# Performance work log

Measured on AMD Instinct MI355X. Metric: run time of the kernel, lower is better.

Reference implementation:

```python
import jax, jax.numpy as jnp
import numpy as np

ATT_SIZE = 32
HEAD_NUM = 2


def setup_inputs() -> dict:
    key = jax.random.key(0)
    k_in, k_q, k_k, k_v, k_r = jax.random.split(key, 5)
    B, F, D = 16384, 32, 64
    H = ATT_SIZE * HEAD_NUM  # 64
    inputs = jax.random.normal(k_in, (B, F, D), dtype=jnp.float32)
    W_Query = jax.random.truncated_normal(k_q, -2.0, 2.0, (D, H), dtype=jnp.float32) * 0.05
    W_Key = jax.random.truncated_normal(k_k, -2.0, 2.0, (D, H), dtype=jnp.float32) * 0.05
    W_Value = jax.random.truncated_normal(k_v, -2.0, 2.0, (D, H), dtype=jnp.float32) * 0.05
    W_Res = jax.random.truncated_normal(k_r, -2.0, 2.0, (D, H), dtype=jnp.float32) * 0.05
    return {"inputs": inputs, "W_Query": W_Query, "W_Key": W_Key, "W_Value": W_Value, "W_Res": W_Res}


def reference(inputs, W_Query, W_Key, W_Value, W_Res):
    B, F, D = inputs.shape
    h, a = HEAD_NUM, ATT_SIZE
    # project and reshape to [B, h, F, a]
    q = jnp.einsum('bfd,de->bfe', inputs, W_Query).reshape(B, F, h, a).transpose(0, 2, 1, 3)
    k = jnp.einsum('bfd,de->bfe', inputs, W_Key).reshape(B, F, h, a).transpose(0, 2, 1, 3)
    v = jnp.einsum('bfd,de->bfe', inputs, W_Value).reshape(B, F, h, a).transpose(0, 2, 1, 3)
    # NOTE: original code has NO 1/sqrt(d) scaling
    scores = jnp.einsum('bhqa,bhka->bhqk', q, k)
    attn = jax.nn.softmax(scores, axis=-1)
    out = jnp.einsum('bhqk,bhka->bhqa', attn, v)  # [B, h, F, a]
    out = out.transpose(0, 2, 1, 3).reshape(B, F, h * a)
    out = out + jnp.einsum('bfd,de->bfe', inputs, W_Res)
    return jax.nn.relu(out)
```

## Files before the change

kernel.cpp:

```cpp
#include <hip/hip_runtime.h>


constexpr int kF = 32, kD = 64, kH = 64;

constexpr int XS = 72;
constexpr int QS = 72;
constexpr int VS = 40;
constexpr int PS = 40;

using short8   = __attribute__((ext_vector_type(8))) short;
using float4v  = __attribute__((ext_vector_type(4))) float;
using ushort4v = __attribute__((ext_vector_type(4))) unsigned short;

__device__ __forceinline__ unsigned short f2bf(float x) {
    return __builtin_bit_cast(unsigned short, (__bf16)x);
}
__device__ __forceinline__ float bf2f(unsigned short b) {
    return __uint_as_float((unsigned)b << 16);
}

__global__ void wprep_kernel(const float* __restrict__ Wq, const float* __restrict__ Wk,
                             const float* __restrict__ Wv, const float* __restrict__ Wr,
                             unsigned short* __restrict__ wt) {
    const int m = blockIdx.x;
    const float* __restrict__ W = (m == 0) ? Wq : (m == 1) ? Wk : (m == 2) ? Wv : Wr;
    for (int i = threadIdx.x; i < kD * kH; i += blockDim.x) {
        const int e = i >> 6, d = i & 63;
        wt[m * kD * kH + e * kD + d] = f2bf(W[d * kH + e]);
    }
}

__global__ __launch_bounds__(256)
void interact_mfma(const float* __restrict__ X, const unsigned short* __restrict__ Wt,
                   float* __restrict__ out)
{
    __shared__ __align__(16) unsigned short s_xp[2 * kF * PS];
    __shared__ __align__(16) unsigned short s_q [kF * QS];
    __shared__ __align__(16) unsigned short s_k [kF * QS];
    __shared__ __align__(16) unsigned short s_vt[kH * VS];
    __shared__ __align__(16) unsigned short s_rt[kH * VS];

    const int t    = threadIdx.x;
    const int w    = t >> 6;
    const int lane = t & 63;
    const int quad = lane >> 4;
    const int l    = lane & 15;
    const int b    = blockIdx.x;

    short8 bfrag[4][2];
    {
        const unsigned short* __restrict__ wtm = Wt + w * (kD * kH);
        #pragma unroll
        for (int nt = 0; nt < 4; ++nt)
            #pragma unroll
            for (int ks = 0; ks < 2; ++ks)
                bfrag[nt][ks] =
                    *reinterpret_cast<const short8*>(wtm + (16 * nt + l) * kD + 32 * ks + quad * 8);
    }

    const float* __restrict__ Xb = X + (size_t)b * (kF * kD);
    #pragma unroll
    for (int i = 0; i < 2; ++i) {
        const int idx = i * 256 + t;
        const int f = idx >> 4, c = idx & 15;
        const float4 v = reinterpret_cast<const float4*>(Xb)[idx];
        ushort4v pk = { f2bf(v.x), f2bf(v.y), f2bf(v.z), f2bf(v.w) };
        *reinterpret_cast<ushort4v*>(&s_xp[f * XS + c * 4]) = pk;
    }
    __syncthreads();

    {
        float4v acc[2][4];
        #pragma unroll
        for (int mt = 0; mt < 2; ++mt)
            #pragma unroll
            for (int nt = 0; nt < 4; ++nt)
                acc[mt][nt] = (float4v){0.f, 0.f, 0.f, 0.f};

        short8 afrag[2][2];
        #pragma unroll
        for (int mt = 0; mt < 2; ++mt)
            #pragma unroll
            for (int ks = 0; ks < 2; ++ks)
                afrag[mt][ks] =
                    *reinterpret_cast<const short8*>(&s_xp[(16 * mt + l) * XS + 32 * ks + quad * 8]);

        #pragma unroll
        for (int mt = 0; mt < 2; ++mt)
            #pragma unroll
            for (int nt = 0; nt < 4; ++nt) {
                acc[mt][nt] = __builtin_amdgcn_mfma_f32_16x16x32_bf16(
                    afrag[mt][0], bfrag[nt][0], acc[mt][nt], 0, 0, 0);
                acc[mt][nt] = __builtin_amdgcn_mfma_f32_16x16x32_bf16(
                    afrag[mt][1], bfrag[nt][1], acc[mt][nt], 0, 0, 0);
            }

        if (w < 2) {
            unsigned short* __restrict__ dst = (w == 0) ? s_q : s_k;
            #pragma unroll
            for (int mt = 0; mt < 2; ++mt)
                #pragma unroll
                for (int nt = 0; nt < 4; ++nt)
                    #pragma unroll
                    for (int r = 0; r < 4; ++r)
                        dst[(16 * mt + quad * 4 + r) * QS + 16 * nt + l] = f2bf(acc[mt][nt][r]);
        } else {
            unsigned short* __restrict__ dstT = (w == 2) ? s_vt : s_rt;
            #pragma unroll
            for (int mt = 0; mt < 2; ++mt)
                #pragma unroll
                for (int nt = 0; nt < 4; ++nt) {
                    ushort4v pk = { f2bf(acc[mt][nt][0]), f2bf(acc[mt][nt][1]),
                                    f2bf(acc[mt][nt][2]), f2bf(acc[mt][nt][3]) };
                    *reinterpret_cast<ushort4v*>(
                        &dstT[(16 * nt + l) * VS + 16 * mt + 4 * quad]) = pk;
                }
        }
    }
    __syncthreads();

    const int h  = w >> 1;
    const int mt = w & 1;
    float inv[4];
    {
        const short8 qa =
            *reinterpret_cast<const short8*>(&s_q[(16 * mt + l) * QS + 32 * h + quad * 8]);
        const short8 kb0 =
            *reinterpret_cast<const short8*>(&s_k[(l) * QS + 32 * h + quad * 8]);
        const short8 kb1 =
            *reinterpret_cast<const short8*>(&s_k[(16 + l) * QS + 32 * h + quad * 8]);

        float4v s0 = (float4v){0.f, 0.f, 0.f, 0.f};
        float4v s1 = (float4v){0.f, 0.f, 0.f, 0.f};
        s0 = __builtin_amdgcn_mfma_f32_16x16x32_bf16(qa, kb0, s0, 0, 0, 0);
        s1 = __builtin_amdgcn_mfma_f32_16x16x32_bf16(qa, kb1, s1, 0, 0, 0);

        #pragma unroll
        for (int r = 0; r < 4; ++r) {
            float m = fmaxf(s0[r], s1[r]);
            #pragma unroll
            for (int d = 1; d < 16; d <<= 1) m = fmaxf(m, __shfl_xor(m, d));
            const float e0 = __expf(s0[r] - m);
            const float e1 = __expf(s1[r] - m);
            float sum = e0 + e1;
            #pragma unroll
            for (int d = 1; d < 16; d <<= 1) sum += __shfl_xor(sum, d);
            inv[r] = __builtin_amdgcn_rcpf(sum);
            const int row = 16 * mt + quad * 4 + r;
            s_xp[(h * kF + row) * PS + l]      = f2bf(e0);
            s_xp[(h * kF + row) * PS + 16 + l] = f2bf(e1);
        }
    }

    {
        const short8 pa =
            *reinterpret_cast<const short8*>(&s_xp[(h * kF + 16 * mt + l) * PS + quad * 8]);
        const short8 vb0 =
            *reinterpret_cast<const short8*>(&s_vt[(32 * h + l) * VS + quad * 8]);
        const short8 vb1 =
            *reinterpret_cast<const short8*>(&s_vt[(32 * h + 16 + l) * VS + quad * 8]);

        float4v o0 = (float4v){0.f, 0.f, 0.f, 0.f};
        float4v o1 = (float4v){0.f, 0.f, 0.f, 0.f};
        o0 = __builtin_amdgcn_mfma_f32_16x16x32_bf16(pa, vb0, o0, 0, 0, 0);
        o1 = __builtin_amdgcn_mfma_f32_16x16x32_bf16(pa, vb1, o1, 0, 0, 0);

        const ushort4v rA =
            *reinterpret_cast<const ushort4v*>(&s_rt[(32 * h + l) * VS + 16 * mt + 4 * quad]);
        const ushort4v rB =
            *reinterpret_cast<const ushort4v*>(&s_rt[(32 * h + 16 + l) * VS + 16 * mt + 4 * quad]);

        float* __restrict__ Ob = out + (size_t)b * (kF * kH);
        #pragma unroll
        for (int r = 0; r < 4; ++r) {
            const int f = 16 * mt + quad * 4 + r;
            Ob[f * kH + 32 * h + l]      = fmaxf(o0[r] * inv[r] + bf2f(rA[r]), 0.0f);
            Ob[f * kH + 32 * h + 16 + l] = fmaxf(o1[r] * inv[r] + bf2f(rB[r]), 0.0f);
        }
    }
}

extern "C" void kernel_launch(void* const* d_in, const int* in_sizes, int n_in,
                              void* d_out, int out_size, void* d_ws, size_t ws_size,
                              hipStream_t stream) {
    const float* X  = (const float*)d_in[0];
    const float* Wq = (const float*)d_in[1];
    const float* Wk = (const float*)d_in[2];
    const float* Wv = (const float*)d_in[3];
    const float* Wr = (const float*)d_in[4];
    float* out = (float*)d_out;
    unsigned short* wt = (unsigned short*)d_ws;

    wprep_kernel<<<4, 256, 0, stream>>>(Wq, Wk, Wv, Wr, wt);

    const int B = in_sizes[0] / (kF * kD);
    interact_mfma<<<B, 256, 0, stream>>>(X, wt, out);
}
```

Before: 271.3 us.

## Compute residual projection in registers, drop softmax max, sum rows via MFMA

Each wave now computes its own residual-projection tile directly into registers, using per-wave fragments of W_Res. This removes the shared-memory round trip for the transposed residual and spreads that projection across all four waves instead of one. Softmax no longer subtracts the row max or does shuffle reductions. The row sums come from an extra MFMA against a ones vector, and the normalization is applied in the epilogue. Skipping the max subtraction removes the shuffle chains, but exp can overflow when scores are large, so it depends on the scale of the inputs.

```diff
diff --git a/kernel.cpp b/kernel.cpp
--- a/kernel.cpp
+++ b/kernel.cpp
@@ -38,7 +38,6 @@
     __shared__ __align__(16) unsigned short s_q [kF * QS];
     __shared__ __align__(16) unsigned short s_k [kF * QS];
     __shared__ __align__(16) unsigned short s_vt[kH * VS];
-    __shared__ __align__(16) unsigned short s_rt[kH * VS];
 
     const int t    = threadIdx.x;
     const int w    = t >> 6;
@@ -46,9 +45,11 @@
     const int quad = lane >> 4;
     const int l    = lane & 15;
     const int b    = blockIdx.x;
+    const int h    = w >> 1;
+    const int wmt  = w & 1;
 
     short8 bfrag[4][2];
-    {
+    if (w < 3) {
         const unsigned short* __restrict__ wtm = Wt + w * (kD * kH);
         #pragma unroll
         for (int nt = 0; nt < 4; ++nt)
@@ -56,6 +57,16 @@
             for (int ks = 0; ks < 2; ++ks)
                 bfrag[nt][ks] =
                     *reinterpret_cast<const short8*>(wtm + (16 * nt + l) * kD + 32 * ks + quad * 8);
+    }
+    short8 rfrag[2][2];
+    {
+        const unsigned short* __restrict__ wtr = Wt + 3 * (kD * kH);
+        #pragma unroll
+        for (int j = 0; j < 2; ++j)
+            #pragma unroll
+            for (int ks = 0; ks < 2; ++ks)
+                rfrag[j][ks] = *reinterpret_cast<const short8*>(
+                    wtr + (16 * (2 * h + j) + l) * kD + 32 * ks + quad * 8);
     }
 
     const float* __restrict__ Xb = X + (size_t)b * (kF * kD);
@@ -69,21 +80,31 @@
     }
     __syncthreads();
 
-    {
+    short8 afrag[2][2];
+    #pragma unroll
+    for (int mt = 0; mt < 2; ++mt)
+        #pragma unroll
+        for (int ks = 0; ks < 2; ++ks)
+            afrag[mt][ks] =
+                *reinterpret_cast<const short8*>(&s_xp[(16 * mt + l) * XS + 32 * ks + quad * 8]);
+
+    float4v accr[2];
+    accr[0] = (float4v){0.f, 0.f, 0.f, 0.f};
+    accr[1] = (float4v){0.f, 0.f, 0.f, 0.f};
+    #pragma unroll
+    for (int j = 0; j < 2; ++j)
+        #pragma unroll
+        for (int ks = 0; ks < 2; ++ks)
+            accr[j] = __builtin_amdgcn_mfma_f32_16x16x32_bf16(
+                afrag[wmt][ks], rfrag[j][ks], accr[j], 0, 0, 0);
+
+    if (w < 3) {
         float4v acc[2][4];
         #pragma unroll
         for (int mt = 0; mt < 2; ++mt)
             #pragma unroll
             for (int nt = 0; nt < 4; ++nt)
                 acc[mt][nt] = (float4v){0.f, 0.f, 0.f, 0.f};
-
-        short8 afrag[2][2];
-        #pragma unroll
-        for (int mt = 0; mt < 2; ++mt)
-            #pragma unroll
-            for (int ks = 0; ks < 2; ++ks)
-                afrag[mt][ks] =
-                    *reinterpret_cast<const short8*>(&s_xp[(16 * mt + l) * XS + 32 * ks + quad * 8]);
 
         #pragma unroll
         for (int mt = 0; mt < 2; ++mt)
@@ -95,7 +116,17 @@
                     afrag[mt][1], bfrag[nt][1], acc[mt][nt], 0, 0, 0);
             }
 
-        if (w < 2) {
+        if (w == 2) {
+            #pragma unroll
+            for (int mt = 0; mt < 2; ++mt)
+                #pragma unroll
+                for (int nt = 0; nt < 4; ++nt) {
+                    ushort4v pk = { f2bf(acc[mt][nt][0]), f2bf(acc[mt][nt][1]),
+                                    f2bf(acc[mt][nt][2]), f2bf(acc[mt][nt][3]) };
+                    *reinterpret_cast<ushort4v*>(
+                        &s_vt[(16 * nt + l) * VS + 16 * mt + 4 * quad]) = pk;
+                }
+        } else {
             unsigned short* __restrict__ dst = (w == 0) ? s_q : s_k;
             #pragma unroll
             for (int mt = 0; mt < 2; ++mt)
@@ -104,27 +135,13 @@
                     #pragma unroll
                     for (int r = 0; r < 4; ++r)
                         dst[(16 * mt + quad * 4 + r) * QS + 16 * nt + l] = f2bf(acc[mt][nt][r]);
-        } else {
-            unsigned short* __restrict__ dstT = (w == 2) ? s_vt : s_rt;
-            #pragma unroll
-            for (int mt = 0; mt < 2; ++mt)
-                #pragma unroll
-                for (int nt = 0; nt < 4; ++nt) {
-                    ushort4v pk = { f2bf(acc[mt][nt][0]), f2bf(acc[mt][nt][1]),
-                                    f2bf(acc[mt][nt][2]), f2bf(acc[mt][nt][3]) };
-                    *reinterpret_cast<ushort4v*>(
-                        &dstT[(16 * nt + l) * VS + 16 * mt + 4 * quad]) = pk;
-                }
         }
     }
     __syncthreads();
 
-    const int h  = w >> 1;
-    const int mt = w & 1;
-    float inv[4];
     {
         const short8 qa =
-            *reinterpret_cast<const short8*>(&s_q[(16 * mt + l) * QS + 32 * h + quad * 8]);
+            *reinterpret_cast<const short8*>(&s_q[(16 * wmt + l) * QS + 32 * h + quad * 8]);
         const short8 kb0 =
             *reinterpret_cast<const short8*>(&s_k[(l) * QS + 32 * h + quad * 8]);
         const short8 kb1 =
@@ -137,45 +154,35 @@
 
         #pragma unroll
         for (int r = 0; r < 4; ++r) {
-            float m = fmaxf(s0[r], s1[r]);
-            #pragma unroll
-            for (int d = 1; d < 16; d <<= 1) m = fmaxf(m, __shfl_xor(m, d));
-            const float e0 = __expf(s0[r] - m);
-            const float e1 = __expf(s1[r] - m);
-            float sum = e0 + e1;
-            #pragma unroll
-            for (int d = 1; d < 16; d <<= 1) sum += __shfl_xor(sum, d);
-            inv[r] = __builtin_amdgcn_rcpf(sum);
-            const int row = 16 * mt + quad * 4 + r;
-            s_xp[(h * kF + row) * PS + l]      = f2bf(e0);
-            s_xp[(h * kF + row) * PS + 16 + l] = f2bf(e1);
+            const int row = 16 * wmt + quad * 4 + r;
+            s_xp[(h * kF + row) * PS + l]      = f2bf(__expf(s0[r]));
+            s_xp[(h * kF + row) * PS + 16 + l] = f2bf(__expf(s1[r]));
         }
     }
 
     {
         const short8 pa =
-            *reinterpret_cast<const short8*>(&s_xp[(h * kF + 16 * mt + l) * PS + quad * 8]);
+            *reinterpret_cast<const short8*>(&s_xp[(h * kF + 16 * wmt + l) * PS + quad * 8]);
         const short8 vb0 =
             *reinterpret_cast<const short8*>(&s_vt[(32 * h + l) * VS + quad * 8]);
         const short8 vb1 =
             *reinterpret_cast<const short8*>(&s_vt[(32 * h + 16 + l) * VS + quad * 8]);
+        const short8 ones = (short8)(short)0x3F80;
 
         float4v o0 = (float4v){0.f, 0.f, 0.f, 0.f};
         float4v o1 = (float4v){0.f, 0.f, 0.f, 0.f};
+        float4v os = (float4v){0.f, 0.f, 0.f, 0.f};
         o0 = __builtin_amdgcn_mfma_f32_16x16x32_bf16(pa, vb0, o0, 0, 0, 0);
         o1 = __builtin_amdgcn_mfma_f32_16x16x32_bf16(pa, vb1, o1, 0, 0, 0);
-
-        const ushort4v rA =
-            *reinterpret_cast<const ushort4v*>(&s_rt[(32 * h + l) * VS + 16 * mt + 4 * quad]);
-        const ushort4v rB =
-            *reinterpret_cast<const ushort4v*>(&s_rt[(32 * h + 16 + l) * VS + 16 * mt + 4 * quad]);
+        os = __builtin_amdgcn_mfma_f32_16x16x32_bf16(pa, ones, os, 0, 0, 0);
 
         float* __restrict__ Ob = out + (size_t)b * (kF * kH);
         #pragma unroll
         for (int r = 0; r < 4; ++r) {
-            const int f = 16 * mt + quad * 4 + r;
-            Ob[f * kH + 32 * h + l]      = fmaxf(o0[r] * inv[r] + bf2f(rA[r]), 0.0f);
-            Ob[f * kH + 32 * h + 16 + l] = fmaxf(o1[r] * inv[r] + bf2f(rB[r]), 0.0f);
+            const int f = 16 * wmt + quad * 4 + r;
+            const float inv = __builtin_amdgcn_rcpf(os[r]);
+            Ob[f * kH + 32 * h + l]      = fmaxf(o0[r] * inv + accr[0][r], 0.0f);
+            Ob[f * kH + 32 * h + 16 + l] = fmaxf(o1[r] * inv + accr[1][r], 0.0f);
         }
     }
 }
```

Result: slower. 323.7 us (+19.3%).
